# Kernel tuning notes

Hardware: AMD Instinct MI355X
Metric: run time of the kernel (lower is better)

The kernel has to match this reference:

```python
import jax, jax.numpy as jnp
import numpy as np

N_NODES = 50000
N_EDGES = 800000
NEG_SLOPE = 0.2


def gat_conv(x, W, al, ar, b, src, dst, num_nodes):
    # x: [N, Din]; W: [Din, H*Dout]; al/ar: [H, Dout]; b: [H*Dout]
    H, Dout = al.shape
    h = (x @ W).reshape(num_nodes, H, Dout)            # [N, H, Dout]
    el = jnp.sum(h * al[None], axis=-1)                # [N, H]
    er = jnp.sum(h * ar[None], axis=-1)                # [N, H]
    e = jax.nn.leaky_relu(el[src] + er[dst], NEG_SLOPE)  # [E, H]
    # segment softmax over incoming edges of each dst node
    m = jax.ops.segment_max(e, dst, num_segments=num_nodes)
    m = jnp.where(jnp.isfinite(m), m, 0.0)
    ex = jnp.exp(e - m[dst])                           # [E, H]
    s = jax.ops.segment_sum(ex, dst, num_segments=num_nodes)
    alpha = ex / s[dst]                                # [E, H]
    msg = h[src] * alpha[:, :, None]                   # [E, H, Dout]
    out = jax.ops.segment_sum(msg, dst, num_segments=num_nodes)
    return out + b.reshape(1, H, Dout)                 # [N, H, Dout]


def setup_inputs() -> dict:
    key = jax.random.key(0)
    ks = jax.random.split(key, 12)
    d_in, hid, heads = 128, 128, 2
    inp = {
        "embedding": jax.random.normal(ks[0], (N_NODES, d_in), jnp.float32),
        "W0": jax.random.normal(ks[1], (d_in, heads * hid), jnp.float32) * 0.1,
        "al0": jax.random.normal(ks[2], (heads, hid), jnp.float32) * 0.1,
        "ar0": jax.random.normal(ks[3], (heads, hid), jnp.float32) * 0.1,
        "b0": jnp.zeros((heads * hid,), jnp.float32),
        "W1": jax.random.normal(ks[4], (heads * hid, heads * hid), jnp.float32) * 0.1,
        "al1": jax.random.normal(ks[5], (1, heads * hid), jnp.float32) * 0.1,
        "ar1": jax.random.normal(ks[6], (1, heads * hid), jnp.float32) * 0.1,
        "b1": jnp.zeros((heads * hid,), jnp.float32),
        "src": jax.random.randint(ks[7], (N_EDGES,), 0, N_NODES, jnp.int32),
        "dst": jax.random.randint(ks[8], (N_EDGES,), 0, N_NODES, jnp.int32),
    }
    return inp


def reference(embedding, W0, al0, ar0, b0, W1, al1, ar1, b1, src, dst):
    n = embedding.shape[0]
    # layer 0: 2 heads, then flatten heads and ReLU (dropout no-op in eval)
    x = gat_conv(embedding, W0, al0, ar0, b0, src, dst, n)  # [N, 2, 128]
    x = jax.nn.relu(x.reshape(n, -1))                        # [N, 256]
    # layer 1: 1 head, squeeze
    x = gat_conv(x, W1, al1, ar1, b1, src, dst, n)           # [N, 1, 256]
    x = x.reshape(n, -1)
    x = x.at[0].set(0.0)
    return x
```

## Files before the change

kernel.cpp:

```cpp
#include <hip/hip_runtime.h>


typedef __attribute__((ext_vector_type(8))) short short8v;
typedef __attribute__((ext_vector_type(4))) float f32x4;

#define LOG2E 1.4426950408889634f

__device__ inline unsigned short f2bf(float x) {
    union { float f; unsigned int u; } v; v.f = x;
    unsigned int r = v.u + 0x7fffu + ((v.u >> 16) & 1u);
    return (unsigned short)(r >> 16);
}
__device__ inline float bf2f(unsigned short h) {
    union { unsigned int u; float f; } v; v.u = ((unsigned int)h) << 16;
    return v.f;
}

template<int H>
__global__ __launch_bounds__(256) void gemm_fused(
    const unsigned short* __restrict__ A, const unsigned short* __restrict__ Bt,
    unsigned short* __restrict__ C,
    const float* __restrict__ al, const float* __restrict__ ar,
    float* __restrict__ el, float* __restrict__ er,
    int M, int N, int K)
{
    __shared__ __align__(16) unsigned short As[128 * 64];
    __shared__ __align__(16) unsigned short Bs[128 * 64];
    const int tid = threadIdx.x;
    const int lane = tid & 63, wv = tid >> 6;
    const int rowBase = blockIdx.x * 128;
    const int colBase = blockIdx.y * 128;

    f32x4 acc[2][8];
    #pragma unroll
    for (int i = 0; i < 2; ++i)
        #pragma unroll
        for (int j = 0; j < 8; ++j)
            acc[i][j] = (f32x4){0.f, 0.f, 0.f, 0.f};

    for (int k0 = 0; k0 < K; k0 += 64) {
        #pragma unroll
        for (int c = tid; c < 128 * 8; c += 256) {
            int row = c >> 3, cc = c & 7;
            int gr = rowBase + row; if (gr >= M) gr = M - 1;
            int4 v = *(const int4*)(A + (size_t)gr * K + k0 + cc * 8);
            *(int4*)&As[row * 64 + (cc ^ (row & 7)) * 8] = v;
        }
        #pragma unroll
        for (int c = tid; c < 128 * 8; c += 256) {
            int n2 = c >> 3, cc = c & 7;
            int4 v = *(const int4*)(Bt + (size_t)(colBase + n2) * K + k0 + cc * 8);
            *(int4*)&Bs[n2 * 64 + (cc ^ (n2 & 7)) * 8] = v;
        }
        __syncthreads();

        #pragma unroll
        for (int ks = 0; ks < 64; ks += 32) {
            int kchunk = (ks >> 3) + (lane >> 4);
            short8v af[2], bfr[8];
            #pragma unroll
            for (int fm = 0; fm < 2; ++fm) {
                int ml = wv * 32 + fm * 16 + (lane & 15);
                af[fm] = *(const short8v*)&As[ml * 64 + (kchunk ^ (ml & 7)) * 8];
            }
            #pragma unroll
            for (int fi = 0; fi < 8; ++fi) {
                int nl = fi * 16 + (lane & 15);
                bfr[fi] = *(const short8v*)&Bs[nl * 64 + (kchunk ^ (nl & 7)) * 8];
            }
            #pragma unroll
            for (int fm = 0; fm < 2; ++fm)
                #pragma unroll
                for (int fi = 0; fi < 8; ++fi)
                    acc[fm][fi] = __builtin_amdgcn_mfma_f32_16x16x32_bf16(
                        af[fm], bfr[fi], acc[fm][fi], 0, 0, 0);
        }
        __syncthreads();
    }

    float alv[8], arv[8];
    #pragma unroll
    for (int fi = 0; fi < 8; ++fi) {
        int col = colBase + fi * 16 + (lane & 15);
        alv[fi] = al[col];
        arv[fi] = ar[col];
    }
    const int head = (H == 2) ? (colBase >> 7) : 0;

    #pragma unroll
    for (int fm = 0; fm < 2; ++fm) {
        #pragma unroll
        for (int r = 0; r < 4; ++r) {
            int row = rowBase + wv * 32 + fm * 16 + (lane >> 4) * 4 + r;
            float pe = 0.f, pr2 = 0.f;
            #pragma unroll
            for (int fi = 0; fi < 8; ++fi) {
                pe  = fmaf(acc[fm][fi][r], alv[fi], pe);
                pr2 = fmaf(acc[fm][fi][r], arv[fi], pr2);
            }
            #pragma unroll
            for (int off = 8; off; off >>= 1) {
                pe  += __shfl_xor(pe, off);
                pr2 += __shfl_xor(pr2, off);
            }
            if (row < M) {
                #pragma unroll
                for (int fi = 0; fi < 8; ++fi) {
                    int col = colBase + fi * 16 + (lane & 15);
                    C[(size_t)row * N + col] = f2bf(acc[fm][fi][r]);
                }
                if ((lane & 15) == 0) {
                    atomicAdd(&el[row * H + head], pe);
                    atomicAdd(&er[row * H + head], pr2);
                }
            }
        }
    }
}

__global__ void conv_count(const float* __restrict__ W0, unsigned short* __restrict__ W0t,
                           const float* __restrict__ W1, unsigned short* __restrict__ W1t,
                           const float* __restrict__ emb, unsigned short* __restrict__ embb,
                           const int* __restrict__ dst, int* __restrict__ cnt,
                           int nbW, int nbE, int E, int nEmb)
{
    int bid = blockIdx.x;
    if (bid < nbW) {
        int t = bid * 256 + threadIdx.x;
        if (t < 128 * 256) {
            int k = t >> 8, n2 = t & 255;
            W0t[n2 * 128 + k] = f2bf(W0[t]);
        }
        int u = t - 128 * 256;
        if (u >= 0 && u < 256 * 256) {
            int k = u >> 8, n2 = u & 255;
            W1t[n2 * 256 + k] = f2bf(W1[u]);
        }
    } else if (bid < nbW + nbE) {
        int t = (bid - nbW) * 256 + threadIdx.x;
        if (t < E) atomicAdd(&cnt[dst[t]], 1);
    } else {
        int t = ((bid - nbW - nbE) * 256 + threadIdx.x) * 4;
        if (t + 3 < nEmb) {
            float4 v = *(const float4*)(emb + t);
            ushort4 o;
            o.x = f2bf(v.x); o.y = f2bf(v.y); o.z = f2bf(v.z); o.w = f2bf(v.w);
            *(ushort4*)(embb + t) = o;
        }
    }
}

__global__ __launch_bounds__(256) void scan_partial(const int* __restrict__ cnt,
                                                    int* __restrict__ bsum, int n)
{
    int t = threadIdx.x;
    int idx = blockIdx.x * 1024 + t * 4;
    int4 v = make_int4(0, 0, 0, 0);
    if (idx + 3 < n) v = *(const int4*)(cnt + idx);
    else if (idx < n) {
        v.x = cnt[idx];
        if (idx + 1 < n) v.y = cnt[idx + 1];
        if (idx + 2 < n) v.z = cnt[idx + 2];
    }
    int s = v.x + v.y + v.z + v.w;
    #pragma unroll
    for (int off = 32; off; off >>= 1) s += __shfl_xor(s, off);
    __shared__ int ws[4];
    if ((t & 63) == 0) ws[t >> 6] = s;
    __syncthreads();
    if (t == 0) bsum[blockIdx.x] = ws[0] + ws[1] + ws[2] + ws[3];
}

__global__ void scan_bsum(int* __restrict__ bsum, int* __restrict__ row,
                          int nb, int n, int E)
{
    int t = threadIdx.x;
    if (nb <= 64) {
        int v = (t < nb) ? bsum[t] : 0;
        int x = v;
        #pragma unroll
        for (int off = 1; off < 64; off <<= 1) {
            int y = __shfl_up(x, off);
            if (t >= off) x += y;
        }
        if (t < nb) bsum[t] = x - v;
    } else if (t == 0) {
        int run = 0;
        for (int i = 0; i < nb; ++i) { int v = bsum[i]; bsum[i] = run; run += v; }
    }
    if (t == 0) row[n] = E;
}

__global__ __launch_bounds__(256) void scan_final(
    const int* __restrict__ cnt, const int* __restrict__ bsum,
    int* __restrict__ row, int* __restrict__ cursor,
    float* __restrict__ el0, float* __restrict__ er0, int n)
{
    int t = threadIdx.x;
    int lane = t & 63;
    int idx = blockIdx.x * 1024 + t * 4;
    int4 v = make_int4(0, 0, 0, 0);
    if (idx + 3 < n) v = *(const int4*)(cnt + idx);
    else if (idx < n) {
        v.x = cnt[idx];
        if (idx + 1 < n) v.y = cnt[idx + 1];
        if (idx + 2 < n) v.z = cnt[idx + 2];
    }
    int s1 = v.x + v.y, s2 = s1 + v.z, s3 = s2 + v.w;
    int tsum = s3;
    int x = tsum;
    #pragma unroll
    for (int off = 1; off < 64; off <<= 1) {
        int y = __shfl_up(x, off);
        if (lane >= off) x += y;
    }
    int wex = x - tsum;
    __shared__ int ws[4];
    if (lane == 63) ws[t >> 6] = x;
    __syncthreads();
    int off0 = bsum[blockIdx.x];
    for (int w2 = 0; w2 < (t >> 6); ++w2) off0 += ws[w2];
    int e0 = off0 + wex;
    float2 z2 = make_float2(0.f, 0.f);
    if (idx < n)     { row[idx]     = e0;        cursor[idx]     = e0;
                       *(float2*)(el0 + 2*idx)     = z2; *(float2*)(er0 + 2*idx)     = z2; }
    if (idx + 1 < n) { row[idx + 1] = e0 + v.x;  cursor[idx + 1] = e0 + v.x;
                       *(float2*)(el0 + 2*idx + 2) = z2; *(float2*)(er0 + 2*idx + 2) = z2; }
    if (idx + 2 < n) { row[idx + 2] = e0 + s1;   cursor[idx + 2] = e0 + s1;
                       *(float2*)(el0 + 2*idx + 4) = z2; *(float2*)(er0 + 2*idx + 4) = z2; }
    if (idx + 3 < n) { row[idx + 3] = e0 + s2;   cursor[idx + 3] = e0 + s2;
                       *(float2*)(el0 + 2*idx + 6) = z2; *(float2*)(er0 + 2*idx + 6) = z2; }
}

__global__ void fill_kernel(const int* __restrict__ src, const int* __restrict__ dst,
                            int* __restrict__ cursor, int* __restrict__ srcc, int E)
{
    int t = blockIdx.x * blockDim.x + threadIdx.x;
    if (t < E) {
        int pos = atomicAdd(&cursor[dst[t]], 1);
        srcc[pos] = src[t];
    }
}

template<int H>
__global__ __launch_bounds__(256) void agg_kernel(
    const unsigned short* __restrict__ h, const float* __restrict__ el,
    const float* __restrict__ er, float* __restrict__ ecsr,
    const int* __restrict__ srcc, const int* __restrict__ row,
    const float* __restrict__ bias, float* __restrict__ outf,
    unsigned short* __restrict__ outb,
    float* __restrict__ elz, float* __restrict__ erz,
    int n_nodes, int E, int do_relu, int zero0)
{
    int wid = blockIdx.x * 4 + (threadIdx.x >> 6);
    if (wid >= n_nodes) return;
    int lane = threadIdx.x & 63;
    int beg = __builtin_amdgcn_readfirstlane(row[wid]);
    int end = __builtin_amdgcn_readfirstlane(row[wid + 1]);
    const int hsel   = (H == 2) ? (lane >> 5) : 0;
    const int stride = (H == 2) ? 32 : 64;
    const int l0     = (H == 2) ? (lane & 31) : lane;
    float* plane = ecsr + (size_t)hsel * E;
    const float rr = er[wid * H + hsel];

    if (elz && lane == 0) { elz[wid] = 0.f; erz[wid] = 0.f; }

    float m = -1e30f, s = 0.f;
    for (int i = beg + l0; i < end; i += stride) {
        int sn = srcc[i];
        float v = el[sn * H + hsel] + rr;
        float ev = ((v > 0.f) ? v : 0.2f * v) * LOG2E;
        plane[i] = ev;
        float mn = fmaxf(m, ev);
        s = s * exp2f(m - mn) + exp2f(ev - mn);
        m = mn;
    }
    #pragma unroll
    for (int off = (H == 2) ? 16 : 32; off; off >>= 1) {
        float mo = __shfl_xor(m, off);
        float so = __shfl_xor(s, off);
        float mn = fmaxf(m, mo);
        s = s * exp2f(m - mn) + so * exp2f(mo - mn);
        m = mn;
    }
    float r = (s > 0.f) ? 1.f / s : 0.f;
    __threadfence_block();

    float aA0 = 0.f, aA1 = 0.f, aA2 = 0.f, aA3 = 0.f;
    float aB0 = 0.f, aB1 = 0.f, aB2 = 0.f, aB3 = 0.f;
    float aC0 = 0.f, aC1 = 0.f, aC2 = 0.f, aC3 = 0.f;
    float aD0 = 0.f, aD1 = 0.f, aD2 = 0.f, aD3 = 0.f;
    int i = beg;
    for (; i + 3 < end; i += 4) {
        float wa = exp2f(plane[i]     - m);
        float wb = exp2f(plane[i + 1] - m);
        float wc = exp2f(plane[i + 2] - m);
        float wd = exp2f(plane[i + 3] - m);
        int sa = srcc[i], sb = srcc[i + 1], sc2 = srcc[i + 2], sd = srcc[i + 3];
        ushort4 ha = *(const ushort4*)(h + (size_t)sa * 256 + lane * 4);
        ushort4 hb = *(const ushort4*)(h + (size_t)sb * 256 + lane * 4);
        ushort4 hc = *(const ushort4*)(h + (size_t)sc2 * 256 + lane * 4);
        ushort4 hd = *(const ushort4*)(h + (size_t)sd * 256 + lane * 4);
        aA0 = fmaf(wa, bf2f(ha.x), aA0); aB0 = fmaf(wb, bf2f(hb.x), aB0);
        aC0 = fmaf(wc, bf2f(hc.x), aC0); aD0 = fmaf(wd, bf2f(hd.x), aD0);
        aA1 = fmaf(wa, bf2f(ha.y), aA1); aB1 = fmaf(wb, bf2f(hb.y), aB1);
        aC1 = fmaf(wc, bf2f(hc.y), aC1); aD1 = fmaf(wd, bf2f(hd.y), aD1);
        aA2 = fmaf(wa, bf2f(ha.z), aA2); aB2 = fmaf(wb, bf2f(hb.z), aB2);
        aC2 = fmaf(wc, bf2f(hc.z), aC2); aD2 = fmaf(wd, bf2f(hd.z), aD2);
        aA3 = fmaf(wa, bf2f(ha.w), aA3); aB3 = fmaf(wb, bf2f(hb.w), aB3);
        aC3 = fmaf(wc, bf2f(hc.w), aC3); aD3 = fmaf(wd, bf2f(hd.w), aD3);
    }
    for (; i < end; ++i) {
        float wa = exp2f(plane[i] - m);
        int sa = srcc[i];
        ushort4 ha = *(const ushort4*)(h + (size_t)sa * 256 + lane * 4);
        aA0 = fmaf(wa, bf2f(ha.x), aA0);
        aA1 = fmaf(wa, bf2f(ha.y), aA1);
        aA2 = fmaf(wa, bf2f(ha.z), aA2);
        aA3 = fmaf(wa, bf2f(ha.w), aA3);
    }

    float4 b4 = *(const float4*)(bias + lane * 4);
    float o0 = ((aA0 + aB0) + (aC0 + aD0)) * r + b4.x;
    float o1 = ((aA1 + aB1) + (aC1 + aD1)) * r + b4.y;
    float o2 = ((aA2 + aB2) + (aC2 + aD2)) * r + b4.z;
    float o3 = ((aA3 + aB3) + (aC3 + aD3)) * r + b4.w;
    if (do_relu) {
        o0 = fmaxf(o0, 0.f); o1 = fmaxf(o1, 0.f);
        o2 = fmaxf(o2, 0.f); o3 = fmaxf(o3, 0.f);
    }
    if (zero0 && wid == 0) { o0 = o1 = o2 = o3 = 0.f; }
    size_t base = (size_t)wid * 256 + lane * 4;
    if (outb) {
        ushort4 o; o.x = f2bf(o0); o.y = f2bf(o1); o.z = f2bf(o2); o.w = f2bf(o3);
        *(ushort4*)(outb + base) = o;
    } else {
        *(float4*)(outf + base) = make_float4(o0, o1, o2, o3);
    }
}

extern "C" void kernel_launch(void* const* d_in, const int* in_sizes, int n_in,
                              void* d_out, int out_size, void* d_ws, size_t ws_size,
                              hipStream_t stream)
{
    const float* emb = (const float*)d_in[0];
    const float* W0  = (const float*)d_in[1];
    const float* al0 = (const float*)d_in[2];
    const float* ar0 = (const float*)d_in[3];
    const float* b0  = (const float*)d_in[4];
    const float* W1  = (const float*)d_in[5];
    const float* al1 = (const float*)d_in[6];
    const float* ar1 = (const float*)d_in[7];
    const float* b1  = (const float*)d_in[8];
    const int* src   = (const int*)d_in[9];
    const int* dst   = (const int*)d_in[10];
    const int N = in_sizes[0] / 128;
    const int E = in_sizes[9];
    float* outp = (float*)d_out;

    char* w = (char*)d_ws;
    auto alloc = [&](size_t bytes) {
        char* p = w;
        w += (bytes + 255) & ~(size_t)255;
        return p;
    };
    unsigned short* hb  = (unsigned short*)alloc((size_t)N * 256 * 2);
    unsigned short* x1b = (unsigned short*)alloc((size_t)N * 256 * 2);
    unsigned short* embb = x1b;
    float* ecsr = (float*)alloc((size_t)E * 2 * 4);
    int* srcc   = (int*)alloc((size_t)E * 4);
    int* rowp   = (int*)alloc((size_t)(N + 1) * 4);
    float* el0  = (float*)alloc((size_t)N * 2 * 4);
    float* er0  = (float*)alloc((size_t)N * 2 * 4);
    float* el1  = (float*)alloc((size_t)N * 4);
    float* er1  = (float*)alloc((size_t)N * 4);
    int* cnt    = (int*)alloc((size_t)N * 4);
    int* cursor = (int*)alloc((size_t)N * 4);
    int* bsum   = (int*)alloc(1024 * 4);
    unsigned short* W0t = (unsigned short*)alloc(256 * 128 * 2);
    unsigned short* W1t = (unsigned short*)alloc(256 * 256 * 2);

    const int nbScan = (N + 1023) / 1024;
    const int nbW = (128 * 256 + 256 * 256 + 255) / 256;
    const int nbE = (E + 255) / 256;
    const int nEmb = N * 128;
    const int nbEmb = (nEmb / 4 + 255) / 256;

    hipMemsetAsync(cnt, 0, (size_t)N * 4, stream);
    conv_count<<<nbW + nbE + nbEmb, 256, 0, stream>>>(
        W0, W0t, W1, W1t, emb, embb, dst, cnt, nbW, nbE, E, nEmb);
    scan_partial<<<nbScan, 256, 0, stream>>>(cnt, bsum, N);
    scan_bsum<<<1, 64, 0, stream>>>(bsum, rowp, nbScan, N, E);
    scan_final<<<nbScan, 256, 0, stream>>>(cnt, bsum, rowp, cursor, el0, er0, N);
    fill_kernel<<<nbE, 256, 0, stream>>>(src, dst, cursor, srcc, E);

    gemm_fused<2><<<dim3((N + 127) / 128, 2), 256, 0, stream>>>(
        embb, W0t, hb, al0, ar0, el0, er0, N, 256, 128);
    agg_kernel<2><<<(N + 3) / 4, 256, 0, stream>>>(
        hb, el0, er0, ecsr, srcc, rowp, b0, nullptr, x1b, el1, er1, N, E, 1, 0);

    gemm_fused<1><<<dim3((N + 127) / 128, 2), 256, 0, stream>>>(
        x1b, W1t, hb, al1, ar1, el1, er1, N, 256, 256);
    agg_kernel<1><<<(N + 3) / 4, 256, 0, stream>>>(
        hb, el1, er1, ecsr, srcc, rowp, b1, outp, nullptr, nullptr, nullptr, N, E, 0, 1);
}
```

Baseline: 280.0 us.

## Fold block-sum scan into scan_final and fuse CSR fill with layer-0 GEMM

Drops the separate single-block scan_bsum launch: every scan_final block now rescans the block sums in its first wavefront to get its own offset. Merges fill_kernel into the layer-0 GEMM launch as extra blocks, so the atomic CSR fill and the GEMM tiles share one grid. This removes two kernel launches and the serialization between them. In exchange the single-wavefront scan now assumes at most 64 scan blocks (N=50000 gives 49), and the larger fused kernel's shared memory is also allocated for the fill blocks, which can limit their occupancy.

Measured after the change: 289.5 us. 3.4% more time.

```diff
diff --git a/kernel.cpp b/kernel.cpp
--- a/kernel.cpp
+++ b/kernel.cpp
@@ -17,19 +17,19 @@
 }
 
 template<int H>
-__global__ __launch_bounds__(256) void gemm_fused(
+__device__ __forceinline__ void gemm_tile(
     const unsigned short* __restrict__ A, const unsigned short* __restrict__ Bt,
     unsigned short* __restrict__ C,
     const float* __restrict__ al, const float* __restrict__ ar,
     float* __restrict__ el, float* __restrict__ er,
-    int M, int N, int K)
+    int M, int N, int K, int bx, int by)
 {
     __shared__ __align__(16) unsigned short As[128 * 64];
     __shared__ __align__(16) unsigned short Bs[128 * 64];
     const int tid = threadIdx.x;
     const int lane = tid & 63, wv = tid >> 6;
-    const int rowBase = blockIdx.x * 128;
-    const int colBase = blockIdx.y * 128;
+    const int rowBase = bx * 128;
+    const int colBase = by * 128;
 
     f32x4 acc[2][8];
     #pragma unroll
@@ -85,7 +85,7 @@
         alv[fi] = al[col];
         arv[fi] = ar[col];
     }
-    const int head = (H == 2) ? (colBase >> 7) : 0;
+    const int head = (H == 2) ? by : 0;
 
     #pragma unroll
     for (int fm = 0; fm < 2; ++fm) {
@@ -118,6 +118,38 @@
     }
 }
 
+template<int H>
+__global__ __launch_bounds__(256) void gemm_fused(
+    const unsigned short* __restrict__ A, const unsigned short* __restrict__ Bt,
+    unsigned short* __restrict__ C,
+    const float* __restrict__ al, const float* __restrict__ ar,
+    float* __restrict__ el, float* __restrict__ er,
+    int M, int N, int K)
+{
+    gemm_tile<H>(A, Bt, C, al, ar, el, er, M, N, K, blockIdx.x, blockIdx.y);
+}
+
+__global__ __launch_bounds__(256) void gemm0_fill(
+    const unsigned short* __restrict__ A, const unsigned short* __restrict__ Bt,
+    unsigned short* __restrict__ C,
+    const float* __restrict__ al, const float* __restrict__ ar,
+    float* __restrict__ el, float* __restrict__ er,
+    int M, int N, int K, int nbG,
+    const int* __restrict__ src, const int* __restrict__ dst,
+    int* __restrict__ cursor, int* __restrict__ srcc, int E)
+{
+    int bid = blockIdx.x;
+    if (bid < nbG) {
+        gemm_tile<2>(A, Bt, C, al, ar, el, er, M, N, K, bid >> 1, bid & 1);
+    } else {
+        int t = (bid - nbG) * 256 + threadIdx.x;
+        if (t < E) {
+            int pos = atomicAdd(&cursor[dst[t]], 1);
+            srcc[pos] = src[t];
+        }
+    }
+}
+
 __global__ void conv_count(const float* __restrict__ W0, unsigned short* __restrict__ W0t,
                            const float* __restrict__ W1, unsigned short* __restrict__ W1t,
                            const float* __restrict__ emb, unsigned short* __restrict__ embb,
@@ -171,33 +203,27 @@
     if (t == 0) bsum[blockIdx.x] = ws[0] + ws[1] + ws[2] + ws[3];
 }
 
-__global__ void scan_bsum(int* __restrict__ bsum, int* __restrict__ row,
-                          int nb, int n, int E)
-{
-    int t = threadIdx.x;
-    if (nb <= 64) {
-        int v = (t < nb) ? bsum[t] : 0;
-        int x = v;
-        #pragma unroll
-        for (int off = 1; off < 64; off <<= 1) {
-            int y = __shfl_up(x, off);
-            if (t >= off) x += y;
-        }
-        if (t < nb) bsum[t] = x - v;
-    } else if (t == 0) {
-        int run = 0;
-        for (int i = 0; i < nb; ++i) { int v = bsum[i]; bsum[i] = run; run += v; }
-    }
-    if (t == 0) row[n] = E;
-}
-
 __global__ __launch_bounds__(256) void scan_final(
     const int* __restrict__ cnt, const int* __restrict__ bsum,
     int* __restrict__ row, int* __restrict__ cursor,
-    float* __restrict__ el0, float* __restrict__ er0, int n)
+    float* __restrict__ el0, float* __restrict__ er0,
+    int n, int nb, int E)
 {
     int t = threadIdx.x;
     int lane = t & 63;
+    __shared__ int blockOff;
+    if (t < 64) {
+        int v = (t < nb) ? bsum[t] : 0;
+        int x = v;
+        #pragma unroll
+        for (int off = 1; off < 64; off <<= 1) {
+            int y = __shfl_up(x, off);
+            if (lane >= off) x += y;
+        }
+        if (t == (int)blockIdx.x) blockOff = x - v;
+    }
+    if (blockIdx.x == 0 && t == 0) row[n] = E;
+
     int idx = blockIdx.x * 1024 + t * 4;
     int4 v = make_int4(0, 0, 0, 0);
     if (idx + 3 < n) v = *(const int4*)(cnt + idx);
@@ -218,7 +244,7 @@
     __shared__ int ws[4];
     if (lane == 63) ws[t >> 6] = x;
     __syncthreads();
-    int off0 = bsum[blockIdx.x];
+    int off0 = blockOff;
     for (int w2 = 0; w2 < (t >> 6); ++w2) off0 += ws[w2];
     int e0 = off0 + wex;
     float2 z2 = make_float2(0.f, 0.f);
@@ -230,16 +256,6 @@
                        *(float2*)(el0 + 2*idx + 4) = z2; *(float2*)(er0 + 2*idx + 4) = z2; }
     if (idx + 3 < n) { row[idx + 3] = e0 + s2;   cursor[idx + 3] = e0 + s2;
                        *(float2*)(el0 + 2*idx + 6) = z2; *(float2*)(er0 + 2*idx + 6) = z2; }
-}
-
-__global__ void fill_kernel(const int* __restrict__ src, const int* __restrict__ dst,
-                            int* __restrict__ cursor, int* __restrict__ srcc, int E)
-{
-    int t = blockIdx.x * blockDim.x + threadIdx.x;
-    if (t < E) {
-        int pos = atomicAdd(&cursor[dst[t]], 1);
-        srcc[pos] = src[t];
-    }
 }
 
 template<int H>
@@ -385,17 +401,18 @@
     const int nbE = (E + 255) / 256;
     const int nEmb = N * 128;
     const int nbEmb = (nEmb / 4 + 255) / 256;
+    const int nbG = ((N + 127) / 128) * 2;
 
     hipMemsetAsync(cnt, 0, (size_t)N * 4, stream);
     conv_count<<<nbW + nbE + nbEmb, 256, 0, stream>>>(
         W0, W0t, W1, W1t, emb, embb, dst, cnt, nbW, nbE, E, nEmb);
     scan_partial<<<nbScan, 256, 0, stream>>>(cnt, bsum, N);
-    scan_bsum<<<1, 64, 0, stream>>>(bsum, rowp, nbScan, N, E);
-    scan_final<<<nbScan, 256, 0, stream>>>(cnt, bsum, rowp, cursor, el0, er0, N);
-    fill_kernel<<<nbE, 256, 0, stream>>>(src, dst, cursor, srcc, E);
-
-    gemm_fused<2><<<dim3((N + 127) / 128, 2), 256, 0, stream>>>(
-        embb, W0t, hb, al0, ar0, el0, er0, N, 256, 128);
+    scan_final<<<nbScan, 256, 0, stream>>>(cnt, bsum, rowp, cursor,
+                                           el0, er0, N, nbScan, E);
+
+    gemm0_fill<<<nbG + nbE, 256, 0, stream>>>(
+        embb, W0t, hb, al0, ar0, el0, er0, N, 256, 128, nbG,
+        src, dst, cursor, srcc, E);
     agg_kernel<2><<<(N + 3) / 4, 256, 0, stream>>>(
         hb, el0, er0, ecsr, srcc, rowp, b0, nullptr, x1b, el1, er1, N, E, 1, 0);
 
```
